# Kernel tuning notes

Measured on AMD Instinct MI355X. Metric: run time of the kernel, lower is better.

Reference implementation:

```python
import jax, jax.numpy as jnp
import numpy as np

K = 16  # neighbors


def knn(x, k):
    # x: [B,N,C]; returns indices of k nearest points (incl. self) [B,N,k]
    sq = jnp.sum(x * x, axis=-1)
    d = sq[:, :, None] + sq[:, None, :] - 2.0 * jnp.einsum('bnc,bmc->bnm', x, x)
    return jax.lax.top_k(-d, k)[1]


def gather_nbrs(x, idx):
    # x: [B,N,C], idx: [B,N,k] -> [B,N,k,C]
    return jax.vmap(lambda xb, ib: xb[ib])(x, idx)


def bn(x, g, b, m, v):
    # Keras BatchNormalization inference mode, eps=1e-3
    return (x - m) * g * jax.lax.rsqrt(v + 1e-3) + b


def dense(x, w, b):
    # Conv1D(kernel_size=1) == pointwise dense over channels
    return jnp.einsum('bnc,co->bno', x, w) + b


def graph_layer(h, k, lw, lb, cw, cb, relu_out):
    g = gather_nbrs(h, knn(h, k))          # [B,N,k,C]
    m = jnp.max(g, axis=2)                 # [B,N,C] max over neighbors
    m = dense(dense(m, lw, lb), cw, cb)
    return jax.nn.relu(m) if relu_out else m


def setup_inputs():
    key = jax.random.key(0)
    ks = jax.random.split(key, 16)
    B, N = 16, 2048
    inp = {'x': jax.random.normal(ks[0], (B, N, 3), jnp.float32)}
    dims = [('conv1', 12, 12), ('conv2', 12, 64), ('conv3', 64, 64),
            ('g1_lin', 64, 64), ('g1_conv', 64, 128),
            ('g2_lin', 128, 128), ('g2_conv', 128, 1024),
            ('conv4', 1024, 1024), ('conv5', 1024, 512)]
    for j, (name, i, o) in enumerate(dims):
        s = (2.0 / (i + o)) ** 0.5  # glorot-ish
        inp[name + '_w'] = jax.random.normal(ks[j + 1], (i, o), jnp.float32) * s
        inp[name + '_b'] = jnp.zeros((o,), jnp.float32)
    for name, c in [('bn1', 12), ('bn2', 64), ('bn3', 64)]:
        inp[name + '_g'] = jnp.ones((c,), jnp.float32)
        inp[name + '_b'] = jnp.zeros((c,), jnp.float32)
        inp[name + '_m'] = jnp.zeros((c,), jnp.float32)
        inp[name + '_v'] = jnp.ones((c,), jnp.float32)
    return inp


def reference(x, conv1_w, conv1_b, conv2_w, conv2_b, conv3_w, conv3_b,
              g1_lin_w, g1_lin_b, g1_conv_w, g1_conv_b,
              g2_lin_w, g2_lin_b, g2_conv_w, g2_conv_b,
              conv4_w, conv4_b, conv5_w, conv5_b,
              bn1_g, bn1_b, bn1_m, bn1_v,
              bn2_g, bn2_b, bn2_m, bn2_v,
              bn3_g, bn3_b, bn3_m, bn3_v):
    B, N = x.shape[0], x.shape[1]
    kx = gather_nbrs(x, knn(x, K))                        # [B,N,K,3]
    c = kx - jnp.mean(kx, axis=2, keepdims=True)
    cov = jnp.einsum('bnki,bnkj->bnij', c, c)             # [B,N,3,3]
    h = jnp.concatenate([x, cov.reshape(B, N, 9)], axis=2)  # [B,N,12]
    h = jax.nn.relu(bn(dense(h, conv1_w, conv1_b), bn1_g, bn1_b, bn1_m, bn1_v))
    h = jax.nn.relu(bn(dense(h, conv2_w, conv2_b), bn2_g, bn2_b, bn2_m, bn2_v))
    h = jax.nn.relu(bn(dense(h, conv3_w, conv3_b), bn3_g, bn3_b, bn3_m, bn3_v))
    h = graph_layer(h, K, g1_lin_w, g1_lin_b, g1_conv_w, g1_conv_b, True)    # [B,N,128]
    h = graph_layer(h, K, g2_lin_w, g2_lin_b, g2_conv_w, g2_conv_b, False)   # [B,N,1024]
    h = jnp.max(h, axis=1, keepdims=True)                 # [B,1,1024]
    h = jax.nn.relu(dense(h, conv4_w, conv4_b))
    return dense(h, conv5_w, conv5_b)                     # [B,1,512]
```

## Files before the change

kernel.cpp:

```cpp
#include <hip/hip_runtime.h>
#include <cstddef>
#include <cstdint>

#define NPTS 2048

typedef short bf16x8 __attribute__((ext_vector_type(8)));
typedef float f32x4 __attribute__((ext_vector_type(4)));

__device__ __forceinline__ unsigned short f2bf(float f) {
  unsigned u = __builtin_bit_cast(unsigned, f);
  unsigned r = u + 0x7fffu + ((u >> 16) & 1u);
  return (unsigned short)(r >> 16);
}
__device__ __forceinline__ float bf2f(unsigned short s) {
  unsigned u = ((unsigned)s) << 16;
  return __builtin_bit_cast(float, u);
}
__device__ __forceinline__ unsigned f2sort(float f) {
  unsigned u = __builtin_bit_cast(unsigned, f);
  return u ^ (unsigned)(((int)u >> 31) | 0x80000000);
}

__device__ __forceinline__ void pool_insert(uint64_t k, uint64_t& s0, uint64_t& s1,
                                            uint64_t& s2, uint64_t& s3) {
  s3 = k < s3 ? k : s3;
  uint64_t t;
  t = s2 < s3 ? s2 : s3; s3 = s2 < s3 ? s3 : s2; s2 = t;
  t = s1 < s2 ? s1 : s2; s2 = s1 < s2 ? s2 : s1; s1 = t;
  t = s0 < s1 ? s0 : s1; s1 = s0 < s1 ? s1 : s0; s0 = t;
}

__device__ __forceinline__ int mbcnt64(unsigned long long m) {
  return __builtin_amdgcn_mbcnt_hi((unsigned)(m >> 32),
                                   __builtin_amdgcn_mbcnt_lo((unsigned)m, 0));
}

__device__ __forceinline__ float wave_sum_f32(float v) {
#pragma unroll
  for (int s = 1; s < 64; s <<= 1) v += __shfl_xor(v, s, 64);
  return v;
}

__device__ __forceinline__ void ins8(unsigned ku, unsigned ii,
                                     unsigned (&kd)[8], unsigned (&pi)[8]) {
  bool c = ku < kd[7];
  kd[7] = c ? ku : kd[7];
  pi[7] = c ? ii : pi[7];
#pragma unroll
  for (int i = 6; i >= 0; --i) {
    bool s = kd[i + 1] < kd[i];
    unsigned tk = s ? kd[i + 1] : kd[i];
    unsigned tp = s ? pi[i + 1] : pi[i];
    kd[i + 1] = s ? kd[i] : kd[i + 1];
    pi[i + 1] = s ? pi[i] : pi[i + 1];
    kd[i] = tk; pi[i] = tp;
  }
}

__global__ __launch_bounds__(256) void k_knn1_cov(const float* __restrict__ x,
                                                  float* __restrict__ h0) {
  const int b = blockIdx.y;
  const int tid = threadIdx.x;
  const int lane = tid & 63;
  const int w = tid >> 6;
  __shared__ float4 xsq[NPTS];
  const float* xb = x + (size_t)b * NPTS * 3;
  for (int i = tid; i < NPTS; i += 256) {
    float a0 = xb[3 * i], a1 = xb[3 * i + 1], a2 = xb[3 * i + 2];
    xsq[i] = make_float4(a0, a1, a2, fmaf(a0, a0, fmaf(a1, a1, a2 * a2)));
  }
  __syncthreads();
  const int nq = blockIdx.x * 4 + w;
  const float4 q4 = xsq[nq];
  const float sqq = q4.w;
  float d[32];
  uint64_t s0 = ~0ull, s1 = ~0ull, s2 = ~0ull, s3 = ~0ull;
#pragma unroll
  for (int j = 0; j < 32; ++j) {
    float4 v = xsq[j * 64 + lane];
    float dot = q4.x * v.x;
    dot = fmaf(q4.y, v.y, dot);
    dot = fmaf(q4.z, v.z, dot);
    float dd = fmaf(-2.f, dot, sqq + v.w);
    d[j] = dd;
    uint64_t k = ((uint64_t)f2sort(dd) << 32) | (unsigned)(j * 64 + lane);
    pool_insert(k, s0, s1, s2, s3);
  }
  const unsigned h0w = (unsigned)(s0 >> 32), m0i = (unsigned)s0;
  const unsigned h1w = (unsigned)(s1 >> 32), m1i = (unsigned)s1;
  const unsigned h2w = (unsigned)(s2 >> 32), m2i = (unsigned)s2;
  const unsigned h3w = (unsigned)(s3 >> 32), m3i = (unsigned)s3;
  unsigned H = 0;
#pragma unroll 1
  for (int bit = 31; bit >= 0; --bit) {
    unsigned tr = H | (1u << bit);
    int c = __popcll(__ballot(h0w < tr)) + __popcll(__ballot(h1w < tr)) +
            __popcll(__ballot(h2w < tr)) + __popcll(__ballot(h3w < tr));
    if (c < 16) H = tr;
  }
  const int cs = __popcll(__ballot(h0w < H)) + __popcll(__ballot(h1w < H)) +
                 __popcll(__ballot(h2w < H)) + __popcll(__ballot(h3w < H));
  const int rneed = 16 - cs;
  const bool e0 = (h0w == H), e1 = (h1w == H), e2 = (h2w == H), e3 = (h3w == H);
  const int gsz = __popcll(__ballot(e0)) + __popcll(__ballot(e1)) +
                  __popcll(__ballot(e2)) + __popcll(__ballot(e3));
  unsigned I = 0xFFFFFFFFu;
  if (gsz > rneed) {
    unsigned Iv = 0;
#pragma unroll 1
    for (int bit = 10; bit >= 0; --bit) {
      unsigned tr = Iv | (1u << bit);
      int c2 = __popcll(__ballot(e0 && m0i < tr)) + __popcll(__ballot(e1 && m1i < tr)) +
               __popcll(__ballot(e2 && m2i < tr)) + __popcll(__ballot(e3 && m3i < tr));
      if (c2 < rneed) Iv = tr;
    }
    I = Iv;
  }
  const bool sel0 = (h0w < H) | (e0 & (m0i <= I));
  const bool sel1 = (h1w < H) | (e1 & (m1i <= I));
  const bool sel2 = (h2w < H) | (e2 & (m2i <= I));
  const bool sel3 = (h3w < H) | (e3 & (m3i <= I));
  const int nsel = (int)sel0 + sel1 + sel2 + sel3;
  float cxx, cxy, cxz, cyy, cyz, czz;
  if (__ballot(nsel == 4) == 0ull) {
    float4 z = make_float4(0.f, 0.f, 0.f, 0.f);
    float4 v0 = sel0 ? xsq[m0i] : z;
    float4 v1 = sel1 ? xsq[m1i] : z;
    float4 v2 = sel2 ? xsq[m2i] : z;
    float4 v3 = sel3 ? xsq[m3i] : z;
    float sx = wave_sum_f32(v0.x + v1.x + v2.x + v3.x);
    float sy = wave_sum_f32(v0.y + v1.y + v2.y + v3.y);
    float sz = wave_sum_f32(v0.z + v1.z + v2.z + v3.z);
    const float mx = sx * 0.0625f, my = sy * 0.0625f, mz = sz * 0.0625f;
    float w0 = sel0 ? 1.f : 0.f, w1 = sel1 ? 1.f : 0.f;
    float w2 = sel2 ? 1.f : 0.f, w3 = sel3 ? 1.f : 0.f;
    float a0x = v0.x - mx, a0y = v0.y - my, a0z = v0.z - mz;
    float a1x = v1.x - mx, a1y = v1.y - my, a1z = v1.z - mz;
    float a2x = v2.x - mx, a2y = v2.y - my, a2z = v2.z - mz;
    float a3x = v3.x - mx, a3y = v3.y - my, a3z = v3.z - mz;
    float pxx = (w0 * a0x) * a0x + (w1 * a1x) * a1x + (w2 * a2x) * a2x + (w3 * a3x) * a3x;
    float pxy = (w0 * a0x) * a0y + (w1 * a1x) * a1y + (w2 * a2x) * a2y + (w3 * a3x) * a3y;
    float pxz = (w0 * a0x) * a0z + (w1 * a1x) * a1z + (w2 * a2x) * a2z + (w3 * a3x) * a3z;
    float pyy = (w0 * a0y) * a0y + (w1 * a1y) * a1y + (w2 * a2y) * a2y + (w3 * a3y) * a3y;
    float pyz = (w0 * a0y) * a0z + (w1 * a1y) * a1z + (w2 * a2y) * a2z + (w3 * a3y) * a3z;
    float pzz = (w0 * a0z) * a0z + (w1 * a1z) * a1z + (w2 * a2z) * a2z + (w3 * a3z) * a3z;
    cxx = wave_sum_f32(pxx); cxy = wave_sum_f32(pxy); cxz = wave_sum_f32(pxz);
    cyy = wave_sum_f32(pyy); cyz = wave_sum_f32(pyz); czz = wave_sum_f32(pzz);
  } else {
    unsigned mask = 0;
    int widx[16];
#pragma unroll 1
    for (int r = 0; r < 16; ++r) {
      float vmin = 3.4e38f;
      int mmin = 0x7fffffff;
#pragma unroll
      for (int j = 0; j < 32; ++j) {
        bool ok = !((mask >> j) & 1u) && (d[j] < vmin);
        if (ok) { vmin = d[j]; mmin = j * 64 + lane; }
      }
#pragma unroll
      for (int s = 1; s < 64; s <<= 1) {
        float ov = __shfl_xor(vmin, s, 64);
        int om = __shfl_xor(mmin, s, 64);
        if (ov < vmin || (ov == vmin && om < mmin)) { vmin = ov; mmin = om; }
      }
      widx[r] = mmin;
      if (lane == (mmin & 63)) mask |= 1u << (mmin >> 6);
    }
    float sx = 0, sy = 0, sz = 0;
#pragma unroll
    for (int r = 0; r < 16; ++r) {
      float4 v = xsq[widx[r]];
      sx += v.x; sy += v.y; sz += v.z;
    }
    const float mx = sx * 0.0625f, my = sy * 0.0625f, mz = sz * 0.0625f;
    cxx = cxy = cxz = cyy = cyz = czz = 0.f;
#pragma unroll
    for (int r = 0; r < 16; ++r) {
      float4 v = xsq[widx[r]];
      float ax = v.x - mx, ay = v.y - my, az = v.z - mz;
      cxx = fmaf(ax, ax, cxx); cxy = fmaf(ax, ay, cxy); cxz = fmaf(ax, az, cxz);
      cyy = fmaf(ay, ay, cyy); cyz = fmaf(ay, az, cyz); czz = fmaf(az, az, czz);
    }
  }
  if (lane == 0) {
    float* o = h0 + ((size_t)b * NPTS + nq) * 12;
    *(float4*)&o[0] = make_float4(q4.x, q4.y, q4.z, cxx);
    *(float4*)&o[4] = make_float4(cxy, cxz, cxy, cyy);
    *(float4*)&o[8] = make_float4(cyz, cxz, cyz, czz);
  }
}

__global__ __launch_bounds__(256) void k_mlp1(
    const float* __restrict__ h0,
    const float* __restrict__ w1, const float* __restrict__ cb1,
    const float* __restrict__ w2, const float* __restrict__ cb2,
    const float* __restrict__ w3, const float* __restrict__ cb3,
    const float* __restrict__ bn1g, const float* __restrict__ bn1b,
    const float* __restrict__ bn1m, const float* __restrict__ bn1v,
    const float* __restrict__ bn2g, const float* __restrict__ bn2b,
    const float* __restrict__ bn2m, const float* __restrict__ bn2v,
    const float* __restrict__ bn3g, const float* __restrict__ bn3b,
    const float* __restrict__ bn3m, const float* __restrict__ bn3v,
    float* __restrict__ h3out,
    unsigned short* __restrict__ h3hi, unsigned short* __restrict__ h3lo) {
  __shared__ float W1[144], W2[768], W3[4096];
  __shared__ float S1[12], F1[12], S2[64], F2[64], S3[64], F3[64];
  __shared__ float h0s[64][12];
  __shared__ float A2[64][65];
  const int tid = threadIdx.x;
  for (int i = tid; i < 144; i += 256) W1[i] = w1[i];
  for (int i = tid; i < 768; i += 256) W2[i] = w2[i];
  for (int i = tid; i < 4096; i += 256) W3[i] = w3[i];
  if (tid < 12) {
    float s = bn1g[tid] * rsqrtf(bn1v[tid] + 1e-3f);
    S1[tid] = s; F1[tid] = (cb1[tid] - bn1m[tid]) * s + bn1b[tid];
  }
  if (tid < 64) {
    float s2 = bn2g[tid] * rsqrtf(bn2v[tid] + 1e-3f);
    S2[tid] = s2; F2[tid] = (cb2[tid] - bn2m[tid]) * s2 + bn2b[tid];
    float s3 = bn3g[tid] * rsqrtf(bn3v[tid] + 1e-3f);
    S3[tid] = s3; F3[tid] = (cb3[tid] - bn3m[tid]) * s3 + bn3b[tid];
  }
  const int p0 = blockIdx.x * 64;
  for (int i = tid; i < 64 * 12; i += 256)
    h0s[i / 12][i % 12] = h0[(size_t)p0 * 12 + i];
  __syncthreads();
  const int pl = tid >> 2;
  const int q = tid & 3;
  float v1[12];
#pragma unroll
  for (int o = 0; o < 12; ++o) {
    float a = 0.f;
#pragma unroll
    for (int i = 0; i < 12; ++i) a = fmaf(h0s[pl][i], W1[i * 12 + o], a);
    v1[o] = fmaxf(fmaf(a, S1[o], F1[o]), 0.f);
  }
#pragma unroll
  for (int o = 0; o < 16; ++o) {
    int oo = q * 16 + o;
    float a = 0.f;
#pragma unroll
    for (int i = 0; i < 12; ++i) a = fmaf(v1[i], W2[i * 64 + oo], a);
    A2[pl][oo] = fmaxf(fmaf(a, S2[oo], F2[oo]), 0.f);
  }
  __syncthreads();
  float acc[16];
#pragma unroll
  for (int o = 0; o < 16; ++o) acc[o] = 0.f;
  for (int i = 0; i < 64; ++i) {
    float xv = A2[pl][i];
#pragma unroll
    for (int o = 0; o < 16; ++o) acc[o] = fmaf(xv, W3[i * 64 + q * 16 + o], acc[o]);
  }
  float vals[16];
#pragma unroll
  for (int o = 0; o < 16; ++o) {
    int oo = q * 16 + o;
    vals[o] = fmaxf(fmaf(acc[o], S3[oo], F3[oo]), 0.f);
  }
  const size_t rowo = (size_t)(p0 + pl) * 64 + q * 16;
  float* orow = h3out + rowo;
#pragma unroll
  for (int o4 = 0; o4 < 4; ++o4)
    *(float4*)&orow[4 * o4] = make_float4(vals[4 * o4], vals[4 * o4 + 1],
                                          vals[4 * o4 + 2], vals[4 * o4 + 3]);
  bf16x8 hv0, hv1, lv0, lv1;
#pragma unroll
  for (int o = 0; o < 8; ++o) {
    unsigned short hb = f2bf(vals[o]);
    hv0[o] = (short)hb; lv0[o] = (short)f2bf(vals[o] - bf2f(hb));
    unsigned short hb1 = f2bf(vals[8 + o]);
    hv1[o] = (short)hb1; lv1[o] = (short)f2bf(vals[8 + o] - bf2f(hb1));
  }
  *(bf16x8*)&h3hi[rowo] = hv0; *(bf16x8*)&h3hi[rowo + 8] = hv1;
  *(bf16x8*)&h3lo[rowo] = lv0; *(bf16x8*)&h3lo[rowo + 8] = lv1;
}

template <int C>
__global__ __launch_bounds__(256) void k_sqnorm(const float* __restrict__ h,
                                                float* __restrict__ sq) {
  const int p = blockIdx.x * 256 + threadIdx.x;
  const float* row = h + (size_t)p * C;
  float a = 0.f;
#pragma unroll
  for (int i = 0; i < C; ++i) a = fmaf(row[i], row[i], a);
  sq[p] = a;
}

template <int C>
__global__ __launch_bounds__(256, 2) void k_knn_pool(
    const unsigned short* __restrict__ hi, const unsigned short* __restrict__ lo,
    const float* __restrict__ sq, const float* __restrict__ h,
    unsigned short* __restrict__ mhi, unsigned short* __restrict__ mlo,
    int* __restrict__ flags) {
  constexpr int KK = C / 32;
  constexpr int DL = C / 4;
  const int tid = threadIdx.x, lane = tid & 63, w = tid >> 6;
  const int f = blockIdx.x;
  const int g = ((f & 7) << 6) | (f >> 3);
  const int b = g >> 5;
  const int q0 = ((g & 31) * 4 + w) * 16;
  const size_t base = (size_t)b * NPTS * C;
  const float* __restrict__ sqb = sq + (size_t)b * NPTS;
  const int r = lane & 15, g4 = lane >> 4, ks = g4 * 8;
  bf16x8 bh[KK], bl[KK];
#pragma unroll
  for (int k4 = 0; k4 < KK; ++k4) {
    bh[k4] = *(const bf16x8*)&hi[base + (size_t)(q0 + r) * C + k4 * 32 + ks];
    bl[k4] = *(const bf16x8*)&lo[base + (size_t)(q0 + r) * C + k4 * 32 + ks];
  }
  const float sqq = sqb[q0 + r];
  unsigned kdA[8], piA[8], kdB[8], piB[8];
#pragma unroll
  for (int i = 0; i < 8; ++i) {
    kdA[i] = 0xFFFFFFFFu; piA[i] = 0xFFFFFFFFu;
    kdB[i] = 0xFFFFFFFFu; piB[i] = 0xFFFFFFFFu;
  }
#pragma unroll 1
  for (int t = 0; t < 128; ++t) {
    f32x4 acc = (f32x4){0.f, 0.f, 0.f, 0.f};
    const unsigned short* ap_h = hi + base + (size_t)(t * 16 + r) * C + ks;
    const unsigned short* ap_l = lo + base + (size_t)(t * 16 + r) * C + ks;
#pragma unroll
    for (int k4 = 0; k4 < KK; ++k4) {
      bf16x8 ah = *(const bf16x8*)(ap_h + k4 * 32);
      bf16x8 al = *(const bf16x8*)(ap_l + k4 * 32);
      acc = __builtin_amdgcn_mfma_f32_16x16x32_bf16(ah, bh[k4], acc, 0, 0, 0);
      acc = __builtin_amdgcn_mfma_f32_16x16x32_bf16(al, bh[k4], acc, 0, 0, 0);
      acc = __builtin_amdgcn_mfma_f32_16x16x32_bf16(ah, bl[k4], acc, 0, 0, 0);
    }
    float4 sqc = *(const float4*)&sqb[t * 16 + g4 * 4];
    const unsigned ib = (unsigned)(t * 16 + g4 * 4);
    {
      float dd = fmaf(-2.f, acc[0], sqq + sqc.x);
      ins8(f2sort(dd), ib + 0, kdA, piA);
    }
    {
      float dd = fmaf(-2.f, acc[1], sqq + sqc.y);
      ins8(f2sort(dd), ib + 1, kdB, piB);
    }
    {
      float dd = fmaf(-2.f, acc[2], sqq + sqc.z);
      ins8(f2sort(dd), ib + 2, kdA, piA);
    }
    {
      float dd = fmaf(-2.f, acc[3], sqq + sqc.w);
      ins8(f2sort(dd), ib + 3, kdB, piB);
    }
  }
  const float* __restrict__ hbp = h + base;
  int cntA = 0, cntB = 0;
  float gm[DL];
#pragma unroll
  for (int j = 0; j < DL; ++j) gm[j] = -3.4e38f;
#pragma unroll 1
  for (int rr = 0; rr < 16; ++rr) {
    uint64_t kA = ((uint64_t)kdA[0] << 32) | piA[0];
    uint64_t kB = ((uint64_t)kdB[0] << 32) | piB[0];
    uint64_t kc = kA < kB ? kA : kB;
    uint64_t km = kc;
    uint64_t o1 = __shfl_xor((unsigned long long)km, 16, 64);
    km = o1 < km ? o1 : km;
    o1 = __shfl_xor((unsigned long long)km, 32, 64);
    km = o1 < km ? o1 : km;
    const bool exA = (kA == km);
    const bool exB = (kB == km);
    cntA += exA ? 1 : 0;
    cntB += exB ? 1 : 0;
#pragma unroll
    for (int i = 0; i < 7; ++i) {
      kdA[i] = exA ? kdA[i + 1] : kdA[i]; piA[i] = exA ? piA[i + 1] : piA[i];
      kdB[i] = exB ? kdB[i + 1] : kdB[i]; piB[i] = exB ? piB[i + 1] : piB[i];
    }
    kdA[7] = exA ? 0xFFFFFFFFu : kdA[7]; piA[7] = exA ? 0xFFFFFFFFu : piA[7];
    kdB[7] = exB ? 0xFFFFFFFFu : kdB[7]; piB[7] = exB ? 0xFFFFFFFFu : piB[7];
    const unsigned m = (unsigned)km;
    const float* row = hbp + (size_t)m * C + g4 * DL;
#pragma unroll
    for (int j4 = 0; j4 < DL / 4; ++j4) {
      float4 v = *(const float4*)&row[j4 * 4];
      gm[j4 * 4 + 0] = fmaxf(gm[j4 * 4 + 0], v.x);
      gm[j4 * 4 + 1] = fmaxf(gm[j4 * 4 + 1], v.y);
      gm[j4 * 4 + 2] = fmaxf(gm[j4 * 4 + 2], v.z);
      gm[j4 * 4 + 3] = fmaxf(gm[j4 * 4 + 3], v.w);
    }
  }
  const bool of = (cntA == 8) || (cntB == 8);
  unsigned long long bal = __ballot(of);
  unsigned qm = (unsigned)((bal >> r) | (bal >> (r + 16)) | (bal >> (r + 32)) |
                           (bal >> (r + 48)));
  if (g4 == 0) flags[b * NPTS + q0 + r] = (int)(qm & 1u);
  const size_t orow = base + (size_t)(q0 + r) * C + g4 * DL;
#pragma unroll
  for (int j8 = 0; j8 < DL / 8; ++j8) {
    bf16x8 hv, lv;
#pragma unroll
    for (int jj = 0; jj < 8; ++jj) {
      float v = gm[j8 * 8 + jj];
      unsigned short hb = f2bf(v);
      hv[jj] = (short)hb;
      lv[jj] = (short)f2bf(v - bf2f(hb));
    }
    *(bf16x8*)&mhi[orow + j8 * 8] = hv;
    *(bf16x8*)&mlo[orow + j8 * 8] = lv;
  }
}

#define DSTRIDE 2052
template <int C>
__global__ __launch_bounds__(1024, 4) void k_knn_fused(
    const unsigned short* __restrict__ hi, const unsigned short* __restrict__ lo,
    const float* __restrict__ sq, const float* __restrict__ h,
    unsigned short* __restrict__ mhi, unsigned short* __restrict__ mlo,
    const int* __restrict__ flags) {
  __shared__ float dmat[16][DSTRIDE];
  __shared__ unsigned nidx[16][16];
  __shared__ int anyf;
  const int tid = threadIdx.x, lane = tid & 63, w = tid >> 6;
  const int f = blockIdx.x;
  const int g = ((f & 7) << 8) | (f >> 3);
  const int b = g >> 7;
  const int q0 = (g & 127) * 16;
  if (tid == 0) {
    int s = 0;
#pragma unroll 1
    for (int i = 0; i < 16; ++i) s |= flags[b * NPTS + q0 + i];
    anyf = s;
  }
  __syncthreads();
  if (!anyf) return;
  const size_t base = (size_t)b * NPTS * C;
  const float* __restrict__ sqb = sq + (size_t)b * NPTS;
  const int r = lane & 15, ks = (lane >> 4) * 8;
  const unsigned short* Ah = hi + base + (size_t)(q0 + r) * C + ks;
  const unsigned short* Al = lo + base + (size_t)(q0 + r) * C + ks;
  float sqq[4];
#pragma unroll
  for (int r2 = 0; r2 < 4; ++r2) sqq[r2] = sqb[q0 + (lane >> 4) * 4 + r2];
  {
    const int m0 = w * 128;
    const unsigned short* Bh = hi + base + (size_t)(m0 + r) * C + ks;
    const unsigned short* Bl = lo + base + (size_t)(m0 + r) * C + ks;
    f32x4 acc[8];
#pragma unroll
    for (int s = 0; s < 8; ++s) acc[s] = (f32x4){0.f, 0.f, 0.f, 0.f};
#pragma unroll
    for (int kk = 0; kk < C; kk += 32) {
      bf16x8 ah = *(const bf16x8*)(Ah + kk);
      bf16x8 al = *(const bf16x8*)(Al + kk);
#pragma unroll
      for (int s = 0; s < 8; ++s) {
        bf16x8 bhv = *(const bf16x8*)(Bh + (size_t)s * 16 * C + kk);
        bf16x8 blv = *(const bf16x8*)(Bl + (size_t)s * 16 * C + kk);
        acc[s] = __builtin_amdgcn_mfma_f32_16x16x32_bf16(ah, bhv, acc[s], 0, 0, 0);
        acc[s] = __builtin_amdgcn_mfma_f32_16x16x32_bf16(ah, blv, acc[s], 0, 0, 0);
        acc[s] = __builtin_amdgcn_mfma_f32_16x16x32_bf16(al, bhv, acc[s], 0, 0, 0);
      }
    }
#pragma unroll
    for (int s = 0; s < 8; ++s) {
      const int col = m0 + s * 16 + (lane & 15);
      float smc = sqb[col];
#pragma unroll
      for (int r2 = 0; r2 < 4; ++r2)
        dmat[(lane >> 4) * 4 + r2][col] = fmaf(-2.f, acc[s][r2], sqq[r2] + smc);
    }
  }
  __syncthreads();
  const float* __restrict__ hbp = h + base;
  const int q = q0 + w;
  uint64_t s0 = ~0ull, s1 = ~0ull, s2 = ~0ull, s3 = ~0ull;
#pragma unroll
  for (int t = 0; t < 8; ++t) {
    float4 dv = *(const float4*)&dmat[w][t * 256 + 4 * lane];
    const unsigned mb = (unsigned)(t * 256 + 4 * lane);
    pool_insert(((uint64_t)f2sort(dv.x) << 32) | (mb + 0), s0, s1, s2, s3);
    pool_insert(((uint64_t)f2sort(dv.y) << 32) | (mb + 1), s0, s1, s2, s3);
    pool_insert(((uint64_t)f2sort(dv.z) << 32) | (mb + 2), s0, s1, s2, s3);
    pool_insert(((uint64_t)f2sort(dv.w) << 32) | (mb + 3), s0, s1, s2, s3);
  }
  const unsigned h0 = (unsigned)(s0 >> 32), m0i = (unsigned)s0;
  const unsigned h1 = (unsigned)(s1 >> 32), m1i = (unsigned)s1;
  const unsigned h2 = (unsigned)(s2 >> 32), m2i = (unsigned)s2;
  const unsigned h3 = (unsigned)(s3 >> 32), m3i = (unsigned)s3;
  unsigned H = 0;
#pragma unroll 1
  for (int bit = 31; bit >= 0; --bit) {
    unsigned tr = H | (1u << bit);
    int c = __popcll(__ballot(h0 < tr)) + __popcll(__ballot(h1 < tr)) +
            __popcll(__ballot(h2 < tr)) + __popcll(__ballot(h3 < tr));
    if (c < 16) H = tr;
  }
  const int cs = __popcll(__ballot(h0 < H)) + __popcll(__ballot(h1 < H)) +
                 __popcll(__ballot(h2 < H)) + __popcll(__ballot(h3 < H));
  const int rneed = 16 - cs;
  const bool e0 = (h0 == H), e1 = (h1 == H), e2 = (h2 == H), e3 = (h3 == H);
  const int gsz = __popcll(__ballot(e0)) + __popcll(__ballot(e1)) +
                  __popcll(__ballot(e2)) + __popcll(__ballot(e3));
  unsigned I = 0xFFFFFFFFu;
  if (gsz > rneed) {
    unsigned Iv = 0;
#pragma unroll 1
    for (int bit = 10; bit >= 0; --bit) {
      unsigned tr = Iv | (1u << bit);
      int c2 = __popcll(__ballot(e0 && m0i < tr)) + __popcll(__ballot(e1 && m1i < tr)) +
               __popcll(__ballot(e2 && m2i < tr)) + __popcll(__ballot(e3 && m3i < tr));
      if (c2 < rneed) Iv = tr;
    }
    I = Iv;
  }
  const bool sel0 = (h0 < H) | (e0 & (m0i <= I));
  const bool sel1 = (h1 < H) | (e1 & (m1i <= I));
  const bool sel2 = (h2 < H) | (e2 & (m2i <= I));
  const bool sel3 = (h3 < H) | (e3 & (m3i <= I));
  const int nsel = (int)sel0 + sel1 + sel2 + sel3;
  float g0 = -3.4e38f, g1 = -3.4e38f;
  if (__ballot(nsel == 4) == 0ull) {
    unsigned long long bm;
    int bpos = 0;
    bm = __ballot(sel0); if (sel0) nidx[w][bpos + mbcnt64(bm)] = m0i; bpos += __popcll(bm);
    bm = __ballot(sel1); if (sel1) nidx[w][bpos + mbcnt64(bm)] = m1i; bpos += __popcll(bm);
    bm = __ballot(sel2); if (sel2) nidx[w][bpos + mbcnt64(bm)] = m2i; bpos += __popcll(bm);
    bm = __ballot(sel3); if (sel3) nidx[w][bpos + mbcnt64(bm)] = m3i;
#pragma unroll
    for (int rr = 0; rr < 16; ++rr) {
      unsigned m = nidx[w][rr];
      const float* row = hbp + (size_t)m * C;
      g0 = fmaxf(g0, row[lane]);
      if (C == 128) g1 = fmaxf(g1, row[64 + lane]);
    }
  } else {
    unsigned mask = 0u;
#pragma unroll 1
    for (int rr = 0; rr < 16; ++rr) {
      float vmin = 3.4e38f;
      int mmin = 0x7fffffff;
#pragma unroll
      for (int j = 0; j < 32; ++j) {
        const int m = (j >> 2) * 256 + 4 * lane + (j & 3);
        float dj = dmat[w][m];
        bool ok = !((mask >> j) & 1u) && (dj < vmin);
        if (ok) { vmin = dj; mmin = m; }
      }
#pragma unroll
      for (int s = 1; s < 64; s <<= 1) {
        float ov = __shfl_xor(vmin, s, 64);
        int om = __shfl_xor(mmin, s, 64);
        if (ov < vmin || (ov == vmin && om < mmin)) { vmin = ov; mmin = om; }
      }
      if (lane == ((mmin >> 2) & 63)) mask |= 1u << (((mmin >> 8) << 2) | (mmin & 3));
      const float* row = hbp + (size_t)mmin * C;
      g0 = fmaxf(g0, row[lane]);
      if (C == 128) g1 = fmaxf(g1, row[64 + lane]);
    }
  }
  const size_t orow = base + (size_t)q * C;
  unsigned short h0b = f2bf(g0);
  mhi[orow + lane] = h0b;
  mlo[orow + lane] = f2bf(g0 - bf2f(h0b));
  if (C == 128) {
    unsigned short h1b = f2bf(g1);
    mhi[orow + 64 + lane] = h1b;
    mlo[orow + 64 + lane] = f2bf(g1 - bf2f(h1b));
  }
}

__global__ __launch_bounds__(256) void k_combine_t(const float* __restrict__ lw,
                                                   const float* __restrict__ lb,
                                                   const float* __restrict__ cw,
                                                   const float* __restrict__ cb,
                                                   unsigned short* __restrict__ wthi,
                                                   unsigned short* __restrict__ wtlo,
                                                   float* __restrict__ bc, int K, int M) {
  const int id = blockIdx.x * 256 + threadIdx.x;
  if (id < K * M) {
    int i = id / M, o = id % M;
    float a = 0.f;
    for (int k = 0; k < K; ++k) a = fmaf(lw[i * K + k], cw[k * M + o], a);
    unsigned short hb = f2bf(a);
    wthi[(size_t)o * K + i] = hb;
    wtlo[(size_t)o * K + i] = f2bf(a - bf2f(hb));
  }
  if (id < M) {
    float a = cb[id];
    for (int k = 0; k < K; ++k) a = fmaf(lb[k], cw[k * M + id], a);
    bc[id] = a;
  }
}

template <int K, int M>
__global__ __launch_bounds__(256) void k_apply_relu(
    const unsigned short* __restrict__ Ah, const unsigned short* __restrict__ Al,
    const unsigned short* __restrict__ Wh, const unsigned short* __restrict__ Wl,
    const float* __restrict__ bias, float* __restrict__ fout,
    unsigned short* __restrict__ phi, unsigned short* __restrict__ plo) {
  const int tid = threadIdx.x, lane = tid & 63, w = tid >> 6;
  const int q0 = blockIdx.x * 64 + w * 16;
  const int m0 = blockIdx.y * 128;
  const int r = lane & 15, ks = (lane >> 4) * 8;
  const unsigned short* ap_h = Ah + (size_t)(q0 + r) * K + ks;
  const unsigned short* ap_l = Al + (size_t)(q0 + r) * K + ks;
  const unsigned short* bp_h = Wh + (size_t)(m0 + r) * K + ks;
  const unsigned short* bp_l = Wl + (size_t)(m0 + r) * K + ks;
  f32x4 acc[8];
#pragma unroll
  for (int mt = 0; mt < 8; ++mt) acc[mt] = (f32x4){0.f, 0.f, 0.f, 0.f};
#pragma unroll
  for (int kk = 0; kk < K; kk += 32) {
    bf16x8 ah = *(const bf16x8*)(ap_h + kk);
    bf16x8 al = *(const bf16x8*)(ap_l + kk);
#pragma unroll
    for (int mt = 0; mt < 8; ++mt) {
      bf16x8 bh = *(const bf16x8*)(bp_h + (size_t)mt * 16 * K + kk);
      bf16x8 bl = *(const bf16x8*)(bp_l + (size_t)mt * 16 * K + kk);
      acc[mt] = __builtin_amdgcn_mfma_f32_16x16x32_bf16(ah, bh, acc[mt], 0, 0, 0);
      acc[mt] = __builtin_amdgcn_mfma_f32_16x16x32_bf16(ah, bl, acc[mt], 0, 0, 0);
      acc[mt] = __builtin_amdgcn_mfma_f32_16x16x32_bf16(al, bh, acc[mt], 0, 0, 0);
    }
  }
#pragma unroll
  for (int mt = 0; mt < 8; ++mt) {
    const int col = m0 + mt * 16 + (lane & 15);
    const float bv = bias[col];
#pragma unroll
    for (int r2 = 0; r2 < 4; ++r2) {
      const int row = q0 + (lane >> 4) * 4 + r2;
      float v = fmaxf(acc[mt][r2] + bv, 0.f);
      const size_t idx = (size_t)row * M + col;
      fout[idx] = v;
      unsigned short hb = f2bf(v);
      phi[idx] = hb;
      plo[idx] = f2bf(v - bf2f(hb));
    }
  }
}

#define WSTRIDE 136
__global__ __launch_bounds__(256, 2) void k_apply_colmax(
    const unsigned short* __restrict__ Ah, const unsigned short* __restrict__ Al,
    const unsigned short* __restrict__ Wh, const unsigned short* __restrict__ Wl,
    const float* __restrict__ bias, float* __restrict__ P) {
  constexpr int K = 128, M = 1024;
  __shared__ unsigned short Bh_s[128 * WSTRIDE];
  __shared__ unsigned short Bl_s[128 * WSTRIDE];
  __shared__ float cm[4][128];
  const int tid = threadIdx.x, lane = tid & 63, w = tid >> 6;
  const int rblk = blockIdx.x;
  const int m0 = blockIdx.y * 128;
  const int r = lane & 15, ks = (lane >> 4) * 8;
  for (int i = tid; i < 128 * 16; i += 256) {
    int row = i >> 4, c8 = (i & 15) * 8;
    *(bf16x8*)&Bh_s[row * WSTRIDE + c8] = *(const bf16x8*)&Wh[(size_t)(m0 + row) * K + c8];
    *(bf16x8*)&Bl_s[row * WSTRIDE + c8] = *(const bf16x8*)&Wl[(size_t)(m0 + row) * K + c8];
  }
  __syncthreads();
  const int q0 = rblk * 256 + w * 64;
  f32x4 acc[4][8];
#pragma unroll
  for (int st = 0; st < 4; ++st)
#pragma unroll
    for (int mt = 0; mt < 8; ++mt) acc[st][mt] = (f32x4){0.f, 0.f, 0.f, 0.f};
#pragma unroll
  for (int kk = 0; kk < K; kk += 32) {
    bf16x8 bh[8], bl[8];
#pragma unroll
    for (int mt = 0; mt < 8; ++mt) {
      bh[mt] = *(const bf16x8*)&Bh_s[(mt * 16 + r) * WSTRIDE + ks + kk];
      bl[mt] = *(const bf16x8*)&Bl_s[(mt * 16 + r) * WSTRIDE + ks + kk];
    }
#pragma unroll
    for (int st = 0; st < 4; ++st) {
      const unsigned short* ap_h = Ah + (size_t)(q0 + st * 16 + r) * K + ks + kk;
      const unsigned short* ap_l = Al + (size_t)(q0 + st * 16 + r) * K + ks + kk;
      bf16x8 ah = *(const bf16x8*)ap_h;
      bf16x8 al = *(const bf16x8*)ap_l;
#pragma unroll
      for (int mt = 0; mt < 8; ++mt) {
        acc[st][mt] = __builtin_amdgcn_mfma_f32_16x16x32_bf16(ah, bh[mt], acc[st][mt], 0, 0, 0);
        acc[st][mt] = __builtin_amdgcn_mfma_f32_16x16x32_bf16(ah, bl[mt], acc[st][mt], 0, 0, 0);
        acc[st][mt] = __builtin_amdgcn_mfma_f32_16x16x32_bf16(al, bh[mt], acc[st][mt], 0, 0, 0);
      }
    }
  }
#pragma unroll
  for (int mt = 0; mt < 8; ++mt) {
    float v = -3.4e38f;
#pragma unroll
    for (int st = 0; st < 4; ++st) {
      v = fmaxf(v, fmaxf(fmaxf(acc[st][mt][0], acc[st][mt][1]),
                         fmaxf(acc[st][mt][2], acc[st][mt][3])));
    }
    v = fmaxf(v, __shfl_xor(v, 16, 64));
    v = fmaxf(v, __shfl_xor(v, 32, 64));
    cm[w][mt * 16 + (lane & 15)] = v;
  }
  __syncthreads();
  if (tid < 128) {
    float m = fmaxf(fmaxf(cm[0][tid], cm[1][tid]), fmaxf(cm[2][tid], cm[3][tid]));
    P[(size_t)rblk * M + m0 + tid] = m + bias[m0 + tid];
  }
}

__global__ __launch_bounds__(256) void k_reduce_max(const float* __restrict__ P,
                                                    float* __restrict__ gmax) {
  const int b = blockIdx.x, tid = threadIdx.x;
  for (int c = tid; c < 1024; c += 256) {
    float m = P[(size_t)(b * 8) * 1024 + c];
    for (int rt = 1; rt < 8; ++rt)
      m = fmaxf(m, P[(size_t)(b * 8 + rt) * 1024 + c]);
    gmax[b * 1024 + c] = m;
  }
}

__global__ __launch_bounds__(256) void k_head1(const float* __restrict__ gmax,
                                               const float* __restrict__ w4,
                                               const float* __restrict__ b4,
                                               float* __restrict__ hid) {
  const int b = blockIdx.y, c0 = blockIdx.x * 64;
  const int tid = threadIdx.x;
  const int c = tid & 63, iq = tid >> 6;
  __shared__ float xs[1024];
  __shared__ float red[4][64];
  for (int i = tid; i < 1024; i += 256) xs[i] = gmax[b * 1024 + i];
  __syncthreads();
  float a = 0.f;
  for (int i = iq * 256; i < iq * 256 + 256; ++i)
    a = fmaf(xs[i], w4[(size_t)i * 1024 + c0 + c], a);
  red[iq][c] = a;
  __syncthreads();
  if (tid < 64) {
    float v = red[0][tid] + red[1][tid] + red[2][tid] + red[3][tid];
    hid[b * 1024 + c0 + tid] = fmaxf(v + b4[c0 + tid], 0.f);
  }
}

__global__ __launch_bounds__(256) void k_head2(const float* __restrict__ hid,
                                               const float* __restrict__ w5,
                                               const float* __restrict__ b5,
                                               float* __restrict__ out) {
  const int b = blockIdx.y, c0 = blockIdx.x * 64;
  const int tid = threadIdx.x;
  const int c = tid & 63, iq = tid >> 6;
  __shared__ float xs[1024];
  __shared__ float red[4][64];
  for (int i = tid; i < 1024; i += 256) xs[i] = hid[b * 1024 + i];
  __syncthreads();
  float a = 0.f;
  for (int i = iq * 256; i < iq * 256 + 256; ++i)
    a = fmaf(xs[i], w5[(size_t)i * 512 + c0 + c], a);
  red[iq][c] = a;
  __syncthreads();
  if (tid < 64) {
    float v = red[0][tid] + red[1][tid] + red[2][tid] + red[3][tid];
    out[(size_t)b * 512 + c0 + tid] = v + b5[c0 + tid];
  }
}

extern "C" void kernel_launch(void* const* d_in, const int* in_sizes, int n_in,
                              void* d_out, int out_size, void* d_ws, size_t ws_size,
                              hipStream_t stream) {
  (void)in_sizes; (void)n_in; (void)out_size; (void)ws_size;
  const float* x = (const float*)d_in[0];
  const float* w1 = (const float*)d_in[1];  const float* b1 = (const float*)d_in[2];
  const float* w2 = (const float*)d_in[3];  const float* b2 = (const float*)d_in[4];
  const float* w3 = (const float*)d_in[5];  const float* b3 = (const float*)d_in[6];
  const float* g1lw = (const float*)d_in[7];  const float* g1lb = (const float*)d_in[8];
  const float* g1cw = (const float*)d_in[9];  const float* g1cb = (const float*)d_in[10];
  const float* g2lw = (const float*)d_in[11]; const float* g2lb = (const float*)d_in[12];
  const float* g2cw = (const float*)d_in[13]; const float* g2cb = (const float*)d_in[14];
  const float* w4 = (const float*)d_in[15]; const float* b4 = (const float*)d_in[16];
  const float* w5 = (const float*)d_in[17]; const float* b5 = (const float*)d_in[18];
  const float* bn1g = (const float*)d_in[19]; const float* bn1b = (const float*)d_in[20];
  const float* bn1m = (const float*)d_in[21]; const float* bn1v = (const float*)d_in[22];
  const float* bn2g = (const float*)d_in[23]; const float* bn2b = (const float*)d_in[24];
  const float* bn2m = (const float*)d_in[25]; const float* bn2v = (const float*)d_in[26];
  const float* bn3g = (const float*)d_in[27]; const float* bn3b = (const float*)d_in[28];
  const float* bn3m = (const float*)d_in[29]; const float* bn3v = (const float*)d_in[30];

  float* ws = (float*)d_ws;
  size_t off = 0;
  auto alloc = [&](size_t n) { float* p = ws + off; off += (n + 63) & ~(size_t)63; return p; };
  float* slotA = alloc(16u * 2048 * 128);
  float* slotB = alloc(16u * 2048 * 64);
  float* sqv  = alloc(16u * 2048);
  unsigned short* hi_h = (unsigned short*)alloc(16u * 2048 * 64);
  unsigned short* lo_h = (unsigned short*)alloc(16u * 2048 * 64);
  unsigned short* mhi = (unsigned short*)alloc(16u * 2048 * 64);
  unsigned short* mlo = (unsigned short*)alloc(16u * 2048 * 64);
  unsigned short* wthi = (unsigned short*)alloc(65536);
  unsigned short* wtlo = (unsigned short*)alloc(65536);
  float* bc   = alloc(1024);
  float* P    = alloc(128u * 1024);
  float* gm   = alloc(16u * 1024);
  float* hid  = alloc(16u * 1024);
  int* flags  = (int*)alloc(16u * 2048);

  k_knn1_cov<<<dim3(512, 16), 256, 0, stream>>>(x, slotA);
  k_mlp1<<<512, 256, 0, stream>>>(slotA, w1, b1, w2, b2, w3, b3,
                                  bn1g, bn1b, bn1m, bn1v,
                                  bn2g, bn2b, bn2m, bn2v,
                                  bn3g, bn3b, bn3m, bn3v, slotB, hi_h, lo_h);
  k_sqnorm<64><<<128, 256, 0, stream>>>(slotB, sqv);
  k_knn_pool<64><<<512, 256, 0, stream>>>(hi_h, lo_h, sqv, slotB, mhi, mlo, flags);
  k_knn_fused<64><<<2048, 1024, 0, stream>>>(hi_h, lo_h, sqv, slotB, mhi, mlo, flags);
  k_combine_t<<<32, 256, 0, stream>>>(g1lw, g1lb, g1cw, g1cb, wthi, wtlo, bc, 64, 128);
  k_apply_relu<64, 128><<<dim3(512, 1), 256, 0, stream>>>(
      mhi, mlo, wthi, wtlo, bc, slotA, hi_h, lo_h);
  k_sqnorm<128><<<128, 256, 0, stream>>>(slotA, sqv);
  k_knn_pool<128><<<512, 256, 0, stream>>>(hi_h, lo_h, sqv, slotA, mhi, mlo, flags);
  k_knn_fused<128><<<2048, 1024, 0, stream>>>(hi_h, lo_h, sqv, slotA, mhi, mlo, flags);
  k_combine_t<<<512, 256, 0, stream>>>(g2lw, g2lb, g2cw, g2cb, wthi, wtlo, bc, 128, 1024);
  k_apply_colmax<<<dim3(128, 8), 256, 0, stream>>>(mhi, mlo, wthi, wtlo, bc, P);
  k_reduce_max<<<16, 256, 0, stream>>>(P, gm);
  k_head1<<<dim3(16, 16), 256, 0, stream>>>(gm, w4, b4, hid);
  k_head2<<<dim3(8, 16), 256, 0, stream>>>(hid, w5, b5, (float*)d_out);
}
```

Baseline: 815.7 us.

## Split KNN candidate scan into two halves with separate merge-and-pool kernel

The KNN pooling kernel now scans only half of the candidate points per block, doubling the grid. Each half writes its partial top-16 keys and overflow flags to a workspace buffer. A new merge kernel combines the two halves per query with wave-wide min reductions and performs the neighbor gather and max-pool. This is meant to raise parallelism and occupancy (launch bounds raised to 4) for the MFMA distance scan, at the cost of an extra launch and global round-trip for the partial top-k lists.

```diff
diff --git a/kernel.cpp b/kernel.cpp
--- a/kernel.cpp
+++ b/kernel.cpp
@@ -39,6 +39,15 @@
 #pragma unroll
   for (int s = 1; s < 64; s <<= 1) v += __shfl_xor(v, s, 64);
   return v;
+}
+
+__device__ __forceinline__ uint64_t wave_min_u64(uint64_t k) {
+#pragma unroll
+  for (int s = 1; s < 64; s <<= 1) {
+    uint64_t ok = __shfl_xor((unsigned long long)k, s, 64);
+    k = ok < k ? ok : k;
+  }
+  return k;
 }
 
 __device__ __forceinline__ void ins8(unsigned ku, unsigned ii,
@@ -289,18 +298,19 @@
 }
 
 template <int C>
-__global__ __launch_bounds__(256, 2) void k_knn_pool(
+__global__ __launch_bounds__(256, 4) void k_knn_pool_half(
     const unsigned short* __restrict__ hi, const unsigned short* __restrict__ lo,
-    const float* __restrict__ sq, const float* __restrict__ h,
-    unsigned short* __restrict__ mhi, unsigned short* __restrict__ mlo,
-    int* __restrict__ flags) {
+    const float* __restrict__ sq, uint64_t* __restrict__ topk,
+    int* __restrict__ flags2) {
   constexpr int KK = C / 32;
-  constexpr int DL = C / 4;
   const int tid = threadIdx.x, lane = tid & 63, w = tid >> 6;
   const int f = blockIdx.x;
-  const int g = ((f & 7) << 6) | (f >> 3);
-  const int b = g >> 5;
-  const int q0 = ((g & 31) * 4 + w) * 16;
+  const int g = ((f & 7) << 7) | (f >> 3);
+  const int b = g >> 6;
+  const int t6 = g & 63;
+  const int half = t6 & 1;
+  const int q0 = ((t6 >> 1) * 4 + w) * 16;
+  const int cb0 = half * 1024;
   const size_t base = (size_t)b * NPTS * C;
   const float* __restrict__ sqb = sq + (size_t)b * NPTS;
   const int r = lane & 15, g4 = lane >> 4, ks = g4 * 8;
@@ -318,10 +328,11 @@
     kdB[i] = 0xFFFFFFFFu; piB[i] = 0xFFFFFFFFu;
   }
 #pragma unroll 1
-  for (int t = 0; t < 128; ++t) {
+  for (int t = 0; t < 64; ++t) {
+    const int ct = cb0 + t * 16;
     f32x4 acc = (f32x4){0.f, 0.f, 0.f, 0.f};
-    const unsigned short* ap_h = hi + base + (size_t)(t * 16 + r) * C + ks;
-    const unsigned short* ap_l = lo + base + (size_t)(t * 16 + r) * C + ks;
+    const unsigned short* ap_h = hi + base + (size_t)(ct + r) * C + ks;
+    const unsigned short* ap_l = lo + base + (size_t)(ct + r) * C + ks;
 #pragma unroll
     for (int k4 = 0; k4 < KK; ++k4) {
       bf16x8 ah = *(const bf16x8*)(ap_h + k4 * 32);
@@ -330,8 +341,8 @@
       acc = __builtin_amdgcn_mfma_f32_16x16x32_bf16(al, bh[k4], acc, 0, 0, 0);
       acc = __builtin_amdgcn_mfma_f32_16x16x32_bf16(ah, bl[k4], acc, 0, 0, 0);
     }
-    float4 sqc = *(const float4*)&sqb[t * 16 + g4 * 4];
-    const unsigned ib = (unsigned)(t * 16 + g4 * 4);
+    float4 sqc = *(const float4*)&sqb[ct + g4 * 4];
+    const unsigned ib = (unsigned)(ct + g4 * 4);
     {
       float dd = fmaf(-2.f, acc[0], sqq + sqc.x);
       ins8(f2sort(dd), ib + 0, kdA, piA);
@@ -349,17 +360,13 @@
       ins8(f2sort(dd), ib + 3, kdB, piB);
     }
   }
-  const float* __restrict__ hbp = h + base;
+  uint64_t* topkq = topk + (((size_t)b * NPTS + q0 + r) * 2 + half) * 16;
   int cntA = 0, cntB = 0;
-  float gm[DL];
-#pragma unroll
-  for (int j = 0; j < DL; ++j) gm[j] = -3.4e38f;
 #pragma unroll 1
   for (int rr = 0; rr < 16; ++rr) {
     uint64_t kA = ((uint64_t)kdA[0] << 32) | piA[0];
     uint64_t kB = ((uint64_t)kdB[0] << 32) | piB[0];
-    uint64_t kc = kA < kB ? kA : kB;
-    uint64_t km = kc;
+    uint64_t km = kA < kB ? kA : kB;
     uint64_t o1 = __shfl_xor((unsigned long long)km, 16, 64);
     km = o1 < km ? o1 : km;
     o1 = __shfl_xor((unsigned long long)km, 32, 64);
@@ -375,35 +382,48 @@
     }
     kdA[7] = exA ? 0xFFFFFFFFu : kdA[7]; piA[7] = exA ? 0xFFFFFFFFu : piA[7];
     kdB[7] = exB ? 0xFFFFFFFFu : kdB[7]; piB[7] = exB ? 0xFFFFFFFFu : piB[7];
-    const unsigned m = (unsigned)km;
-    const float* row = hbp + (size_t)m * C + g4 * DL;
-#pragma unroll
-    for (int j4 = 0; j4 < DL / 4; ++j4) {
-      float4 v = *(const float4*)&row[j4 * 4];
-      gm[j4 * 4 + 0] = fmaxf(gm[j4 * 4 + 0], v.x);
-      gm[j4 * 4 + 1] = fmaxf(gm[j4 * 4 + 1], v.y);
-      gm[j4 * 4 + 2] = fmaxf(gm[j4 * 4 + 2], v.z);
-      gm[j4 * 4 + 3] = fmaxf(gm[j4 * 4 + 3], v.w);
-    }
+    if (g4 == 0) topkq[rr] = km;
   }
   const bool of = (cntA == 8) || (cntB == 8);
   unsigned long long bal = __ballot(of);
   unsigned qm = (unsigned)((bal >> r) | (bal >> (r + 16)) | (bal >> (r + 32)) |
                            (bal >> (r + 48)));
-  if (g4 == 0) flags[b * NPTS + q0 + r] = (int)(qm & 1u);
-  const size_t orow = base + (size_t)(q0 + r) * C + g4 * DL;
-#pragma unroll
-  for (int j8 = 0; j8 < DL / 8; ++j8) {
-    bf16x8 hv, lv;
-#pragma unroll
-    for (int jj = 0; jj < 8; ++jj) {
-      float v = gm[j8 * 8 + jj];
-      unsigned short hb = f2bf(v);
-      hv[jj] = (short)hb;
-      lv[jj] = (short)f2bf(v - bf2f(hb));
-    }
-    *(bf16x8*)&mhi[orow + j8 * 8] = hv;
-    *(bf16x8*)&mlo[orow + j8 * 8] = lv;
+  if (g4 == 0) flags2[((b * NPTS + q0 + r) << 1) | half] = (int)(qm & 1u);
+}
+
+template <int C>
+__global__ __launch_bounds__(256, 4) void k_knn_merge(
+    const uint64_t* __restrict__ topk, const int* __restrict__ flags2,
+    const float* __restrict__ h, unsigned short* __restrict__ mhi,
+    unsigned short* __restrict__ mlo, int* __restrict__ flags) {
+  const int tid = threadIdx.x, lane = tid & 63, w = tid >> 6;
+  const int f = blockIdx.x;
+  const int g = ((f & 7) << 10) | (f >> 3);
+  const int b = g >> 9;
+  const int q = (g & 511) * 4 + w;
+  const size_t qi = (size_t)b * NPTS + q;
+  uint64_t k = ~0ull;
+  if (lane < 32) k = topk[(qi * 2 + (lane >> 4)) * 16 + (lane & 15)];
+  if (lane == 0) flags[qi] = flags2[qi << 1] | flags2[(qi << 1) | 1];
+  const float* __restrict__ hbp = h + (size_t)b * NPTS * C;
+  float g0 = -3.4e38f, g1 = -3.4e38f;
+#pragma unroll 1
+  for (int rr = 0; rr < 16; ++rr) {
+    uint64_t km = wave_min_u64(k);
+    if (k == km) k = ~0ull;
+    const unsigned m = (unsigned)km;
+    const float* row = hbp + (size_t)m * C;
+    g0 = fmaxf(g0, row[lane]);
+    if (C == 128) g1 = fmaxf(g1, row[64 + lane]);
+  }
+  const size_t orow = (size_t)b * NPTS * C + (size_t)q * C;
+  unsigned short h0b = f2bf(g0);
+  mhi[orow + lane] = h0b;
+  mlo[orow + lane] = f2bf(g0 - bf2f(h0b));
+  if (C == 128) {
+    unsigned short h1b = f2bf(g1);
+    mhi[orow + 64 + lane] = h1b;
+    mlo[orow + 64 + lane] = f2bf(g1 - bf2f(h1b));
   }
 }
 
@@ -795,6 +815,8 @@
   float* gm   = alloc(16u * 1024);
   float* hid  = alloc(16u * 1024);
   int* flags  = (int*)alloc(16u * 2048);
+  int* flags2 = (int*)alloc(16u * 2048 * 2);
+  uint64_t* topk = (uint64_t*)alloc(16u * 2048 * 2 * 16 * 2);
 
   k_knn1_cov<<<dim3(512, 16), 256, 0, stream>>>(x, slotA);
   k_mlp1<<<512, 256, 0, stream>>>(slotA, w1, b1, w2, b2, w3, b3,
@@ -802,13 +824,15 @@
                                   bn2g, bn2b, bn2m, bn2v,
                                   bn3g, bn3b, bn3m, bn3v, slotB, hi_h, lo_h);
   k_sqnorm<64><<<128, 256, 0, stream>>>(slotB, sqv);
-  k_knn_pool<64><<<512, 256, 0, stream>>>(hi_h, lo_h, sqv, slotB, mhi, mlo, flags);
+  k_knn_pool_half<64><<<1024, 256, 0, stream>>>(hi_h, lo_h, sqv, topk, flags2);
+  k_knn_merge<64><<<8192, 256, 0, stream>>>(topk, flags2, slotB, mhi, mlo, flags);
   k_knn_fused<64><<<2048, 1024, 0, stream>>>(hi_h, lo_h, sqv, slotB, mhi, mlo, flags);
   k_combine_t<<<32, 256, 0, stream>>>(g1lw, g1lb, g1cw, g1cb, wthi, wtlo, bc, 64, 128);
   k_apply_relu<64, 128><<<dim3(512, 1), 256, 0, stream>>>(
       mhi, mlo, wthi, wtlo, bc, slotA, hi_h, lo_h);
   k_sqnorm<128><<<128, 256, 0, stream>>>(slotA, sqv);
-  k_knn_pool<128><<<512, 256, 0, stream>>>(hi_h, lo_h, sqv, slotA, mhi, mlo, flags);
+  k_knn_pool_half<128><<<1024, 256, 0, stream>>>(hi_h, lo_h, sqv, topk, flags2);
+  k_knn_merge<128><<<8192, 256, 0, stream>>>(topk, flags2, slotA, mhi, mlo, flags);
   k_knn_fused<128><<<2048, 1024, 0, stream>>>(hi_h, lo_h, sqv, slotA, mhi, mlo, flags);
   k_combine_t<<<512, 256, 0, stream>>>(g2lw, g2lb, g2cw, g2cb, wthi, wtlo, bc, 128, 1024);
   k_apply_colmax<<<dim3(128, 8), 256, 0, stream>>>(mhi, mlo, wthi, wtlo, bc, P);
```

New measurement: 931.9 us. 14.3% more time.
